# Optimization experiments

Hardware: AMD Instinct MI355X
Metric: run time of the kernel (lower is better)

The kernel has to match this reference:

```python
import jax, jax.numpy as jnp
import numpy as np

EMBED = 768
HEADS = 12
HEAD_DIM = EMBED // HEADS
WINDOW_SIZES = (16, 64, 256)
LN_EPS = 1e-5


def setup_inputs() -> dict:
    key = jax.random.key(0)
    ks = jax.random.split(key, 8)
    B, S = 4, 1024
    s = 1.0 / np.sqrt(EMBED)
    return {
        "query": jax.random.normal(ks[0], (B, S, EMBED), dtype=jnp.float32),
        "key": jax.random.normal(ks[1], (B, S, EMBED), dtype=jnp.float32),
        "value": jax.random.normal(ks[2], (B, S, EMBED), dtype=jnp.float32),
        "attention_mask": jnp.ones((B, S), dtype=jnp.float32),
        "Wq": jax.random.normal(ks[3], (EMBED, EMBED), dtype=jnp.float32) * s,
        "bq": jnp.zeros((EMBED,), dtype=jnp.float32),
        "Wk": jax.random.normal(ks[4], (EMBED, EMBED), dtype=jnp.float32) * s,
        "bk": jnp.zeros((EMBED,), dtype=jnp.float32),
        "Wv": jax.random.normal(ks[5], (EMBED, EMBED), dtype=jnp.float32) * s,
        "bv": jnp.zeros((EMBED,), dtype=jnp.float32),
        "window_weights": jnp.ones((len(WINDOW_SIZES),), dtype=jnp.float32) / len(WINDOW_SIZES),
        "gamma": jnp.ones((EMBED,), dtype=jnp.float32),
        "beta": jnp.zeros((EMBED,), dtype=jnp.float32),
    }


def reference(query, key, value, attention_mask, Wq, bq, Wk, bk, Wv, bv,
              window_weights, gamma, beta):
    B, S, _ = query.shape

    def proj(x, W, b):
        # [B,S,E] -> [B,H,S,D]  (torch nn.Linear: x @ W.T + b)
        return (x @ W.T + b).reshape(B, S, HEADS, HEAD_DIM).transpose(0, 2, 1, 3)

    q = proj(query, Wq, bq)
    k = proj(key, Wk, bk)
    v = proj(value, Wv, bv)

    # full [B,H,S,S] scores (dropout in eval mode = identity)
    scores = jnp.einsum("bhqd,bhkd->bhqk", q, k) / np.sqrt(HEAD_DIM)

    idx = jnp.arange(S)
    am = attention_mask[:, None, None, :]  # broadcast over heads and query dim
    combined = jnp.zeros_like(scores)
    for i, w in enumerate(WINDOW_SIZES):
        # band mask |i-j| <= w; note scores are multiplicatively masked
        # and carried across scales, exactly as in the torch loop
        band = (jnp.abs(idx[:, None] - idx[None, :]) <= w).astype(scores.dtype)
        scores = scores * band * am
        combined = combined + window_weights[i] * jax.nn.softmax(scores, axis=-1)

    context = jnp.einsum("bhqk,bhkd->bhqd", combined, v)
    context = context.transpose(0, 2, 1, 3).reshape(B, S, EMBED)
    q_flat = q.transpose(0, 2, 1, 3).reshape(B, S, EMBED)

    x = q_flat + context
    mean = jnp.mean(x, axis=-1, keepdims=True)
    var = jnp.var(x, axis=-1, keepdims=True)
    return gamma * (x - mean) / jnp.sqrt(var + LN_EPS) + beta
```

## Files before the change

### kernel.cpp

```cpp
#include <hip/hip_runtime.h>
#include <hip/hip_bf16.h>

#define EMB   768
#define SEQ   1024
#define NBAT  4
#define MROWS 4096
#define NHEAD 12
#define HD    64
#define WIN   16
#define QB    16
#define KB    64
#define LN_EPS 1e-5f

typedef __attribute__((ext_vector_type(8))) short bf16x8;
typedef __attribute__((ext_vector_type(4))) float f32x4;
typedef unsigned short u16;
typedef unsigned int   u32;

static __device__ inline u16 f2bf(float f) {
    union { float f; u32 u; } a; a.f = f;
    u32 u = a.u;
    u32 r = (u + 0x7fffu + ((u >> 16) & 1u)) >> 16;
    return (u16)r;
}
static __device__ inline float bf2f(u16 x) {
    union { u32 u; float f; } c; c.u = ((u32)x) << 16; return c.f;
}
static __device__ inline u32 cvt2(float lo, float hi) {
    __hip_bfloat162 t = __float22bfloat162_rn(float2{lo, hi});
    union { __hip_bfloat162 h; u32 u; } c; c.h = t; return c.u;
}
static __device__ inline bf16x8 pack8(float4 a, float4 b) {
    union { bf16x8 v; u32 w[4]; } r;
    r.w[0] = cvt2(a.x, a.y); r.w[1] = cvt2(a.z, a.w);
    r.w[2] = cvt2(b.x, b.y); r.w[3] = cvt2(b.z, b.w);
    return r.v;
}

#define WT4  147456u
__global__ __launch_bounds__(256) void cast_w(
    const float* __restrict__ wq, const float* __restrict__ wk, const float* __restrict__ wv,
    u16* __restrict__ Wbf, float* __restrict__ Vsum)
{
    u32 u = blockIdx.x * 256u + threadIdx.x;
    if (u < NBAT * EMB) Vsum[u] = 0.f;
    u32 which = u / WT4;
    u32 off = (u - which * WT4) * 4u;
    const float* src = which == 0 ? wq : (which == 1 ? wk : wv);
    float4 val = *(const float4*)(src + off);
    ushort4 o;
    o.x = f2bf(val.x); o.y = f2bf(val.y); o.z = f2bf(val.z); o.w = f2bf(val.w);
    *(ushort4*)(Wbf + (size_t)which * 589824u + off) = o;
}

#define GK 768
#define GN 768

static __device__ inline void gload_lds16(const void* g, void* l) {
    __builtin_amdgcn_global_load_lds((const __attribute__((address_space(1))) void*)g,
                                     (__attribute__((address_space(3))) void*)l, 16, 0, 0);
}

__global__ __launch_bounds__(256) void gemm_qkv(
    const float* __restrict__ qa, const float* __restrict__ ka, const float* __restrict__ va,
    const u16* __restrict__ Wbase,
    const float* __restrict__ bq, const float* __restrict__ bk, const float* __restrict__ bv,
    u16* __restrict__ Qb, u16* __restrict__ Kb, u16* __restrict__ Vb,
    float* __restrict__ Vsum)
{
    const int z = blockIdx.z;
    const float* Af = (z == 0) ? qa : ((z == 1) ? ka : va);
    const u16* W = Wbase + (size_t)z * (GN * GK);
    const float* bias = (z == 0) ? bq : ((z == 1) ? bk : bv);
    u16* Ob = (z == 0) ? Qb : ((z == 1) ? Kb : Vb);

    int id = blockIdx.y * 6 + blockIdx.x;
    int swz = (id & 7) * 48 + (id >> 3);
    const int bm = (swz / 6) * 64, bn = (swz % 6) * 128;

    const int tid = threadIdx.x, wave = tid >> 6, lane = tid & 63;

    __shared__ __align__(16) u16 As[2][64 * 64];
    __shared__ __align__(16) u16 Bs[2][128 * 64];

    f32x4 acc[2][4];
#pragma unroll
    for (int i = 0; i < 2; ++i)
#pragma unroll
        for (int j = 0; j < 4; ++j) acc[i][j] = (f32x4){0.f, 0.f, 0.f, 0.f};

    const int wr = (wave >> 1) * 32, wc = (wave & 1) * 64;
    const int r0 = lane & 15, hk = lane >> 4;

    const int ar = tid >> 2, ac2 = (tid & 3) * 2;
    const float* arowp = Af + (size_t)(bm + ar) * GK + (tid & 3) * 16;
    const int asw0 = ar * 64 + ((ac2 ^ (ar & 7)) * 8);
    const int asw1 = ar * 64 + (((ac2 + 1) ^ (ar & 7)) * 8);

    int brow[4], bcol[4];
#pragma unroll
    for (int j = 0; j < 4; ++j) {
        int c = j * 256 + tid;
        brow[j] = c >> 3;
        bcol[j] = ((c & 7) ^ (brow[j] & 7)) * 8;
    }

    float4 ae0, ae1, ae2, ae3;
    float4 ao0, ao1, ao2, ao3;

#define STAGE_W(buf, K0) do { \
    _Pragma("unroll") for (int j = 0; j < 4; ++j) \
        gload_lds16(W + (size_t)(bn + brow[j]) * GK + (K0) + bcol[j], \
                    &Bs[buf][(j * 256 + tid) * 8]); \
} while (0)

#define ALOAD_E(K0) do { const float* p = arowp + (K0); \
    ae0 = *(const float4*)p; ae1 = *(const float4*)(p + 4); \
    ae2 = *(const float4*)(p + 8); ae3 = *(const float4*)(p + 12); } while (0)
#define ALOAD_O(K0) do { const float* p = arowp + (K0); \
    ao0 = *(const float4*)p; ao1 = *(const float4*)(p + 4); \
    ao2 = *(const float4*)(p + 8); ao3 = *(const float4*)(p + 12); } while (0)

#define ACVT_E(buf) do { \
    *(bf16x8*)&As[buf][asw0] = pack8(ae0, ae1); \
    *(bf16x8*)&As[buf][asw1] = pack8(ae2, ae3); } while (0)
#define ACVT_O(buf) do { \
    *(bf16x8*)&As[buf][asw0] = pack8(ao0, ao1); \
    *(bf16x8*)&As[buf][asw1] = pack8(ao2, ao3); } while (0)

#define GEMM_COMPUTE(buf) do { \
    bf16x8 af[2][2], bg[2][4]; \
    _Pragma("unroll") for (int kk = 0; kk < 2; ++kk) { \
        _Pragma("unroll") for (int i = 0; i < 2; ++i) { \
            int ra = wr + i * 16 + r0; int sa = (kk * 4 + hk) ^ (ra & 7); \
            af[kk][i] = *(const bf16x8*)&As[buf][ra * 64 + sa * 8]; } \
        _Pragma("unroll") for (int j = 0; j < 4; ++j) { \
            int rb = wc + j * 16 + r0; int sb = (kk * 4 + hk) ^ (rb & 7); \
            bg[kk][j] = *(const bf16x8*)&Bs[buf][rb * 64 + sb * 8]; } } \
    _Pragma("unroll") for (int kk = 0; kk < 2; ++kk) \
    _Pragma("unroll") for (int i = 0; i < 2; ++i) \
    _Pragma("unroll") for (int j = 0; j < 4; ++j) \
        acc[i][j] = __builtin_amdgcn_mfma_f32_16x16x32_bf16(af[kk][i], bg[kk][j], acc[i][j], 0, 0, 0); \
} while (0)

    STAGE_W(0, 0);
    __builtin_amdgcn_sched_barrier(0);
    ALOAD_E(0);
    __builtin_amdgcn_sched_barrier(0);

    for (int t = 0; t < 12; ++t) {
        int cur = t & 1;
        if (t < 11) {
            STAGE_W(cur ^ 1, (t + 1) * 64);
            __builtin_amdgcn_sched_barrier(0);
            if (cur == 0) ALOAD_O((t + 1) * 64);
            else          ALOAD_E((t + 1) * 64);
            __builtin_amdgcn_sched_barrier(0);
        }
        if (cur == 0) ACVT_E(0); else ACVT_O(1);
        asm volatile("s_waitcnt lgkmcnt(0)" ::: "memory");
        __builtin_amdgcn_sched_barrier(0);
        __builtin_amdgcn_s_barrier();
        __builtin_amdgcn_sched_barrier(0);
        GEMM_COMPUTE(cur);
        __builtin_amdgcn_sched_barrier(0);
        __builtin_amdgcn_s_barrier();
        __builtin_amdgcn_sched_barrier(0);
    }

#undef STAGE_W
#undef ALOAD_E
#undef ALOAD_O
#undef ACVT_E
#undef ACVT_O
#undef GEMM_COMPUTE

    const int cl = lane & 15, rb4 = (lane >> 4) * 4;
#pragma unroll
    for (int i = 0; i < 2; ++i)
#pragma unroll
        for (int j = 0; j < 4; ++j) {
            int col = bn + wc + j * 16 + cl;
            float b_ = bias[col];
#pragma unroll
            for (int r = 0; r < 4; ++r) {
                int row = bm + wr + i * 16 + rb4 + r;
                Ob[(size_t)row * GN + col] = f2bf(acc[i][j][r] + b_);
            }
        }

    if (z == 2) {
        const int bb = bm >> 10;
#pragma unroll
        for (int j = 0; j < 4; ++j) {
            int col = bn + wc + j * 16 + cl;
            float s = bias[col] * 8.f;
#pragma unroll
            for (int i = 0; i < 2; ++i)
#pragma unroll
                for (int r = 0; r < 4; ++r) s += acc[i][j][r];
            s += __shfl_xor(s, 16, 64);
            s += __shfl_xor(s, 32, 64);
            if (hk == 0)
                atomicAdd(&Vsum[bb * EMB + col], s);
        }
    }
}

__global__ __launch_bounds__(768, 3) void attn_ln(
    const u16* __restrict__ Qb, const u16* __restrict__ Kb, const u16* __restrict__ Vb,
    const float* __restrict__ Vsum, const float* __restrict__ am, const float* __restrict__ ww,
    const float* __restrict__ gamma, const float* __restrict__ beta, float* __restrict__ out)
{
    int id = blockIdx.x + 64 * blockIdx.y;
    int swz = (id & 7) * 32 + (id >> 3);
    const int qt = swz & 63, b = swz >> 6;

    const int q0 = qt * QB;
    int kstart = q0 - WIN;
    if (kstart < 0) kstart = 0;
    if (kstart > SEQ - KB) kstart = SEQ - KB;

    const int h = threadIdx.x >> 6, lane = threadIdx.x & 63;
    const int fr = lane & 15, hk = lane >> 4;
    const int kof = hk * 8, rowg = hk * 4;

    __shared__ __align__(16) u16 Ps[NHEAD][QB][68];
    __shared__ __align__(16) float xs[QB][772];
    __shared__ float ps1[QB][13], ps2[QB][13];
    __shared__ float mu[QB], rs[QB];

    const float w0 = ww[0], w1 = ww[1], w2 = ww[2];

    bf16x8 aq[2], bk4[4][2], bv4[4][2];
    {
        const u16* qb = Qb + ((size_t)(b * SEQ + q0)) * EMB + h * HD;
#pragma unroll
        for (int kk = 0; kk < 2; ++kk)
            aq[kk] = *(const bf16x8*)(qb + (size_t)fr * EMB + kk * 32 + kof);
        const u16* kb = Kb + ((size_t)(b * SEQ + kstart)) * EMB + h * HD;
#pragma unroll
        for (int nj = 0; nj < 4; ++nj)
#pragma unroll
            for (int kk = 0; kk < 2; ++kk)
                bk4[nj][kk] = *(const bf16x8*)(kb + (size_t)(nj * 16 + fr) * EMB + kk * 32 + kof);
        const u16* vb = Vb + ((size_t)(b * SEQ + kstart)) * EMB + h * HD;
#pragma unroll
        for (int nj = 0; nj < 4; ++nj)
#pragma unroll
            for (int kk = 0; kk < 2; ++kk) {
                union { bf16x8 v; u16 s[8]; } tmp;
#pragma unroll
                for (int j = 0; j < 8; ++j)
                    tmp.s[j] = vb[(size_t)(kk * 32 + kof + j) * EMB + nj * 16 + fr];
                bv4[nj][kk] = tmp.v;
            }
    }

    f32x4 sc[4];
#pragma unroll
    for (int j = 0; j < 4; ++j) sc[j] = (f32x4){0.f, 0.f, 0.f, 0.f};
#pragma unroll
    for (int kk = 0; kk < 2; ++kk)
#pragma unroll
        for (int nj = 0; nj < 4; ++nj)
            sc[nj] = __builtin_amdgcn_mfma_f32_16x16x32_bf16(aq[kk], bk4[nj][kk], sc[nj], 0, 0, 0);

    float amv[4];
#pragma unroll
    for (int nj = 0; nj < 4; ++nj) amv[nj] = am[b * SEQ + kstart + nj * 16 + fr];

    float t[4][4], cj[4][4], ua[4];
#pragma unroll
    for (int nj = 0; nj < 4; ++nj)
#pragma unroll
        for (int r = 0; r < 4; ++r) {
            int qrow = q0 + rowg + r;
            int kcol = kstart + nj * 16 + fr;
            int d = qrow - kcol; if (d < 0) d = -d;
            t[nj][r] = (d <= WIN) ? sc[nj][r] * 0.125f * amv[nj] : 0.f;
            cj[nj][r] = 0.f;
        }
#pragma unroll
    for (int r = 0; r < 4; ++r) ua[r] = 0.f;

#pragma unroll
    for (int it = 0; it < 3; ++it) {
        float wwi = it == 0 ? w0 : (it == 1 ? w1 : w2);
#pragma unroll
        for (int r = 0; r < 4; ++r) {
            float m = 0.f;
#pragma unroll
            for (int nj = 0; nj < 4; ++nj) m = fmaxf(m, t[nj][r]);
#pragma unroll
            for (int o = 1; o < 16; o <<= 1) m = fmaxf(m, __shfl_xor(m, o, 64));
            float e4[4], s = 0.f;
#pragma unroll
            for (int nj = 0; nj < 4; ++nj) { e4[nj] = __expf(t[nj][r] - m); s += e4[nj]; }
#pragma unroll
            for (int o = 1; o < 16; o <<= 1) s += __shfl_xor(s, o, 64);
            float un = __expf(-m);
            s += (float)(SEQ - KB) * un;
            float inv = wwi / s;
#pragma unroll
            for (int nj = 0; nj < 4; ++nj) cj[nj][r] += e4[nj] * inv;
            ua[r] += un * inv;
        }
        if (it < 2) {
#pragma unroll
            for (int nj = 0; nj < 4; ++nj)
#pragma unroll
                for (int r = 0; r < 4; ++r) t[nj][r] *= amv[nj];
        }
    }

#pragma unroll
    for (int nj = 0; nj < 4; ++nj)
#pragma unroll
        for (int r = 0; r < 4; ++r)
            Ps[h][rowg + r][nj * 16 + fr] = f2bf(cj[nj][r] - ua[r]);

    f32x4 pv[4];
#pragma unroll
    for (int j = 0; j < 4; ++j) pv[j] = (f32x4){0.f, 0.f, 0.f, 0.f};
#pragma unroll
    for (int kk = 0; kk < 2; ++kk) {
        bf16x8 ap = *(const bf16x8*)&Ps[h][fr][kk * 32 + kof];
#pragma unroll
        for (int nj = 0; nj < 4; ++nj)
            pv[nj] = __builtin_amdgcn_mfma_f32_16x16x32_bf16(ap, bv4[nj][kk], pv[nj], 0, 0, 0);
    }

    float vs[4];
#pragma unroll
    for (int nj = 0; nj < 4; ++nj) vs[nj] = Vsum[b * EMB + h * HD + nj * 16 + fr];

    float xv[4][4];
#pragma unroll
    for (int nj = 0; nj < 4; ++nj)
#pragma unroll
        for (int r = 0; r < 4; ++r) {
            int row = q0 + rowg + r;
            float qres = bf2f(Qb[((size_t)(b * SEQ + row)) * EMB + h * HD + nj * 16 + fr]);
            xv[nj][r] = qres + pv[nj][r] + ua[r] * vs[nj];
            xs[rowg + r][h * HD + nj * 16 + fr] = xv[nj][r];
        }

    float s1r[4], s2r[4];
#pragma unroll
    for (int r = 0; r < 4; ++r) {
        float a = 0.f, c = 0.f;
#pragma unroll
        for (int nj = 0; nj < 4; ++nj) { a += xv[nj][r]; c += xv[nj][r] * xv[nj][r]; }
#pragma unroll
        for (int o = 1; o < 16; o <<= 1) { a += __shfl_xor(a, o, 64); c += __shfl_xor(c, o, 64); }
        s1r[r] = a; s2r[r] = c;
    }
    if (fr == 0) {
#pragma unroll
        for (int r = 0; r < 4; ++r) { ps1[rowg + r][h] = s1r[r]; ps2[rowg + r][h] = s2r[r]; }
    }
    __syncthreads();
    if (h == 0 && lane < QB) {
        float a = 0.f, c = 0.f;
#pragma unroll
        for (int w = 0; w < NHEAD; ++w) { a += ps1[lane][w]; c += ps2[lane][w]; }
        float mean = a * (1.f / EMB);
        float var = c * (1.f / EMB) - mean * mean;
        mu[lane] = mean;
        rs[lane] = rsqrtf(var + LN_EPS);
    }
    __syncthreads();

    {
        const int tt = threadIdx.x;
        const int rbase = tt / 192, c4 = tt % 192;
        float4 g4 = *(const float4*)(gamma + c4 * 4);
        float4 b4 = *(const float4*)(beta + c4 * 4);
#pragma unroll
        for (int k4 = 0; k4 < 4; ++k4) {
            int row = rbase + k4 * 4;
            float4 x4 = *(const float4*)&xs[row][c4 * 4];
            float m_ = mu[row], r_ = rs[row];
            float4 o;
            o.x = g4.x * (x4.x - m_) * r_ + b4.x;
            o.y = g4.y * (x4.y - m_) * r_ + b4.y;
            o.z = g4.z * (x4.z - m_) * r_ + b4.z;
            o.w = g4.w * (x4.w - m_) * r_ + b4.w;
            *(float4*)(out + ((size_t)(b * SEQ + q0 + row)) * EMB + c4 * 4) = o;
        }
    }
}

extern "C" void kernel_launch(void* const* d_in, const int* in_sizes, int n_in,
                              void* d_out, int out_size, void* d_ws, size_t ws_size,
                              hipStream_t stream)
{
    const float* q     = (const float*)d_in[0];
    const float* k     = (const float*)d_in[1];
    const float* v     = (const float*)d_in[2];
    const float* amask = (const float*)d_in[3];
    const float* Wq    = (const float*)d_in[4];
    const float* bq    = (const float*)d_in[5];
    const float* Wk    = (const float*)d_in[6];
    const float* bk    = (const float*)d_in[7];
    const float* Wv    = (const float*)d_in[8];
    const float* bv    = (const float*)d_in[9];
    const float* ww    = (const float*)d_in[10];
    const float* gamma = (const float*)d_in[11];
    const float* beta  = (const float*)d_in[12];
    float* out = (float*)d_out;

    char* ws = (char*)d_ws;
    u16*   Wbf  = (u16*)(ws);
    u16*   Qbf  = (u16*)(ws + 3538944);
    u16*   Kbf  = (u16*)(ws + 9830400);
    u16*   Vbf  = (u16*)(ws + 16121856);
    float* Vsum = (float*)(ws + 22413312);

    hipLaunchKernelGGL(cast_w, dim3(1728), dim3(256), 0, stream,
                       Wq, Wk, Wv, Wbf, Vsum);
    hipLaunchKernelGGL(gemm_qkv, dim3(GN / 128, MROWS / 64, 3), dim3(256), 0, stream,
                       q, k, v, Wbf, bq, bk, bv, Qbf, Kbf, Vbf, Vsum);
    hipLaunchKernelGGL(attn_ln, dim3(SEQ / QB, NBAT), dim3(768), 0, stream,
                       Qbf, Kbf, Vbf, Vsum, amask, ww, gamma, beta, out);
}
```

Baseline: 60.92 us.

## Stage fp32 activations directly into LDS via async loads, convert at fragment read

The QKV projection GEMM previously loaded fp32 activations into registers, packed them to bf16, and stored them to LDS each K step. Now both A (as fp32, swizzled over 16 columns) and W tiles are copied global-to-LDS with direct async loads, waited on with a vmcnt counter, and the bf16 conversion happens when MFMA fragments are read. This removes the register round-trip and the VALU/LDS-store work from the producer side, at the cost of doubling A's LDS footprint and LDS read traffic, and of repeating the conversion for every wave that reads the same data.

```diff
diff --git a/kernel.cpp b/kernel.cpp
--- a/kernel.cpp
+++ b/kernel.cpp
@@ -80,8 +80,8 @@
 
     const int tid = threadIdx.x, wave = tid >> 6, lane = tid & 63;
 
-    __shared__ __align__(16) u16 As[2][64 * 64];
-    __shared__ __align__(16) u16 Bs[2][128 * 64];
+    __shared__ __align__(16) float Asf[2][64 * 64];
+    __shared__ __align__(16) u16   Bs[2][128 * 64];
 
     f32x4 acc[2][4];
 #pragma unroll
@@ -92,48 +92,57 @@
     const int wr = (wave >> 1) * 32, wc = (wave & 1) * 64;
     const int r0 = lane & 15, hk = lane >> 4;
 
-    const int ar = tid >> 2, ac2 = (tid & 3) * 2;
-    const float* arowp = Af + (size_t)(bm + ar) * GK + (tid & 3) * 16;
-    const int asw0 = ar * 64 + ((ac2 ^ (ar & 7)) * 8);
-    const int asw1 = ar * 64 + (((ac2 + 1) ^ (ar & 7)) * 8);
-
-    int brow[4], bcol[4];
+    int asrow[4], ascol[4];
 #pragma unroll
     for (int j = 0; j < 4; ++j) {
         int c = j * 256 + tid;
+        asrow[j] = c >> 4;
+        ascol[j] = ((c & 15) ^ (asrow[j] & 15)) * 4;
+    }
+    int brow[4], bcol[4];
+#pragma unroll
+    for (int j = 0; j < 4; ++j) {
+        int c = (j & 1) * 256 + tid;
         brow[j] = c >> 3;
         bcol[j] = ((c & 7) ^ (brow[j] & 7)) * 8;
     }
 
-    float4 ae0, ae1, ae2, ae3;
-    float4 ao0, ao1, ao2, ao3;
-
-#define STAGE_W(buf, K0) do { \
+#define GEMM_STAGE(buf, K0) do { \
+    _Pragma("unroll") for (int j = 0; j < 4; ++j) \
+        gload_lds16(Af + (size_t)(bm + asrow[j]) * GK + (K0) + ascol[j], \
+                    &Asf[buf][(j * 256 + tid) * 4]); \
     _Pragma("unroll") for (int j = 0; j < 4; ++j) \
         gload_lds16(W + (size_t)(bn + brow[j]) * GK + (K0) + bcol[j], \
-                    &Bs[buf][(j * 256 + tid) * 8]); \
+                    &Bs[buf][((j & 1) * 256 + tid) * 8 + (j >> 1) * 4096]); \
 } while (0)
-
-#define ALOAD_E(K0) do { const float* p = arowp + (K0); \
-    ae0 = *(const float4*)p; ae1 = *(const float4*)(p + 4); \
-    ae2 = *(const float4*)(p + 8); ae3 = *(const float4*)(p + 12); } while (0)
-#define ALOAD_O(K0) do { const float* p = arowp + (K0); \
-    ao0 = *(const float4*)p; ao1 = *(const float4*)(p + 4); \
-    ao2 = *(const float4*)(p + 8); ao3 = *(const float4*)(p + 12); } while (0)
-
-#define ACVT_E(buf) do { \
-    *(bf16x8*)&As[buf][asw0] = pack8(ae0, ae1); \
-    *(bf16x8*)&As[buf][asw1] = pack8(ae2, ae3); } while (0)
-#define ACVT_O(buf) do { \
-    *(bf16x8*)&As[buf][asw0] = pack8(ao0, ao1); \
-    *(bf16x8*)&As[buf][asw1] = pack8(ao2, ao3); } while (0)
+#undef GEMM_STAGE
+#define GEMM_STAGE(buf, K0) do { \
+    _Pragma("unroll") for (int j = 0; j < 4; ++j) \
+        gload_lds16(Af + (size_t)(bm + asrow[j]) * GK + (K0) + ascol[j], \
+                    &Asf[buf][(j * 256 + tid) * 4]); \
+    _Pragma("unroll") for (int j = 0; j < 2; ++j) { \
+        int c = j * 256 + tid; \
+        int rw = c >> 3; \
+        int cw = ((c & 7) ^ (rw & 7)) * 8; \
+        gload_lds16(W + (size_t)(bn + rw) * GK + (K0) + cw, \
+                    &Bs[buf][c * 8]); \
+        int c2 = c + 512; \
+        int rw2 = c2 >> 3; \
+        int cw2 = ((c2 & 7) ^ (rw2 & 7)) * 8; \
+        gload_lds16(W + (size_t)(bn + rw2) * GK + (K0) + cw2, \
+                    &Bs[buf][c2 * 8]); } \
+} while (0)
 
 #define GEMM_COMPUTE(buf) do { \
     bf16x8 af[2][2], bg[2][4]; \
     _Pragma("unroll") for (int kk = 0; kk < 2; ++kk) { \
         _Pragma("unroll") for (int i = 0; i < 2; ++i) { \
-            int ra = wr + i * 16 + r0; int sa = (kk * 4 + hk) ^ (ra & 7); \
-            af[kk][i] = *(const bf16x8*)&As[buf][ra * 64 + sa * 8]; } \
+            int ra = wr + i * 16 + r0; \
+            int cb = kk * 8 + hk * 2; \
+            int sa0 = cb ^ (ra & 15), sa1 = (cb + 1) ^ (ra & 15); \
+            float4 f0 = *(const float4*)&Asf[buf][ra * 64 + sa0 * 4]; \
+            float4 f1 = *(const float4*)&Asf[buf][ra * 64 + sa1 * 4]; \
+            af[kk][i] = pack8(f0, f1); } \
         _Pragma("unroll") for (int j = 0; j < 4; ++j) { \
             int rb = wc + j * 16 + r0; int sb = (kk * 4 + hk) ^ (rb & 7); \
             bg[kk][j] = *(const bf16x8*)&Bs[buf][rb * 64 + sb * 8]; } } \
@@ -143,22 +152,11 @@
         acc[i][j] = __builtin_amdgcn_mfma_f32_16x16x32_bf16(af[kk][i], bg[kk][j], acc[i][j], 0, 0, 0); \
 } while (0)
 
-    STAGE_W(0, 0);
-    __builtin_amdgcn_sched_barrier(0);
-    ALOAD_E(0);
-    __builtin_amdgcn_sched_barrier(0);
-
-    for (int t = 0; t < 12; ++t) {
+    GEMM_STAGE(0, 0);
+    for (int t = 0; t < 11; ++t) {
         int cur = t & 1;
-        if (t < 11) {
-            STAGE_W(cur ^ 1, (t + 1) * 64);
-            __builtin_amdgcn_sched_barrier(0);
-            if (cur == 0) ALOAD_O((t + 1) * 64);
-            else          ALOAD_E((t + 1) * 64);
-            __builtin_amdgcn_sched_barrier(0);
-        }
-        if (cur == 0) ACVT_E(0); else ACVT_O(1);
-        asm volatile("s_waitcnt lgkmcnt(0)" ::: "memory");
+        GEMM_STAGE(cur ^ 1, (t + 1) * 64);
+        asm volatile("s_waitcnt vmcnt(8)" ::: "memory");
         __builtin_amdgcn_sched_barrier(0);
         __builtin_amdgcn_s_barrier();
         __builtin_amdgcn_sched_barrier(0);
@@ -167,12 +165,13 @@
         __builtin_amdgcn_s_barrier();
         __builtin_amdgcn_sched_barrier(0);
     }
-
-#undef STAGE_W
-#undef ALOAD_E
-#undef ALOAD_O
-#undef ACVT_E
-#undef ACVT_O
+    asm volatile("s_waitcnt vmcnt(0)" ::: "memory");
+    __builtin_amdgcn_sched_barrier(0);
+    __builtin_amdgcn_s_barrier();
+    __builtin_amdgcn_sched_barrier(0);
+    GEMM_COMPUTE(1);
+
+#undef GEMM_STAGE
 #undef GEMM_COMPUTE
 
     const int cl = lane & 15, rb4 = (lane >> 4) * 4;
```

Result: slower. 67.15 us (+10.2%).
